# Kernel tuning notes

Measured on AMD Instinct MI355X. Metric: run time of the kernel, lower is better.

## Reference

```python
import jax, jax.numpy as jnp
import numpy as np

N_HEAD = 16

def setup_inputs() -> dict:
    key = jax.random.key(0)
    k1, k2, k3 = jax.random.split(key, 3)
    B, T, D = 1, 2048, 1024
    x = jax.random.normal(k1, (B, T, D), dtype=jnp.float32)
    # torch Linear(d, 3d, bias=False): y = x @ W.T with W [3d, d]; store transposed [d, 3d]
    W_qkv = jax.random.normal(k2, (D, 3 * D), dtype=jnp.float32) * 0.02
    W_o = jax.random.normal(k3, (D, D), dtype=jnp.float32) * 0.02
    return {"x": x, "W_qkv": W_qkv, "W_o": W_o}

def reference(x, W_qkv, W_o):
    B, T, D = x.shape
    H = N_HEAD
    hd = D // H
    qkv = (x @ W_qkv).reshape(B, T, 3, H, hd)
    q, k, v = qkv[:, :, 0], qkv[:, :, 1], qkv[:, :, 2]  # [B, T, H, hd]
    scale = 1.0 / np.sqrt(hd).astype(np.float32)
    # The per-chunk loop with growing context + mask is exactly dense causal attention.
    att = jnp.einsum('bqhd,bkhd->bhqk', q, k) * scale  # [B, H, T, T]
    causal = jnp.tril(jnp.ones((T, T), dtype=bool))
    att = jnp.where(causal[None, None], att, jnp.finfo(att.dtype).min)
    att = jax.nn.softmax(att, axis=-1)
    y = jnp.einsum('bhqk,bkhd->bqhd', att, v).reshape(B, T, D)
    return y @ W_o
```

## Files before the change

kernel.cpp:

```cpp
#include <hip/hip_runtime.h>
#include <hip/hip_bf16.h>


using u16 = unsigned short;
typedef __attribute__((ext_vector_type(8))) __bf16 bf16x8;
typedef __attribute__((ext_vector_type(8))) unsigned short u16x8;
typedef __attribute__((ext_vector_type(4))) float f32x4;

__device__ __forceinline__ u16 f2bf(float f) {
  union { float f; unsigned u; } v; v.f = f;
  unsigned r = v.u + 0x7FFFu + ((v.u >> 16) & 1u);
  return (u16)(r >> 16);
}

__device__ __forceinline__ float bf2f(u16 b) {
  union { unsigned u; float f; } v; v.u = ((unsigned)b) << 16;
  return v.f;
}

__device__ __forceinline__ unsigned cvt_pk_bf16(float lo, float hi) {
  unsigned r;
  asm("v_cvt_pk_bf16_f32 %0, %1, %2" : "=v"(r) : "v"(lo), "v"(hi));
  return r;
}

__device__ __forceinline__ void gload_lds16(const void* g, void* l) {
  __builtin_amdgcn_global_load_lds((const __attribute__((address_space(1))) void*)g,
                                   (__attribute__((address_space(3))) void*)l, 16, 0, 0);
}

__device__ __forceinline__ f32x4 mfma16(bf16x8 a, bf16x8 b, f32x4 c) {
  return __builtin_amdgcn_mfma_f32_16x16x32_bf16(a, b, c, 0, 0, 0);
}

__global__ __launch_bounds__(256) void prep_kernel(const float* __restrict__ x,
                                                   const float* __restrict__ Wqkv,
                                                   const float* __restrict__ Wo,
                                                   u16* __restrict__ xb,
                                                   u16* __restrict__ WqkvT,
                                                   u16* __restrict__ WoT) {
  __shared__ u16 tile[32][33];
  const int b = blockIdx.x;
  if (b < 1024) {
    const int i = (b * 256 + threadIdx.x) * 8;
    float4 a = *(const float4*)(x + i);
    float4 c = *(const float4*)(x + i + 4);
    u16x8 r;
    r[0] = f2bf(a.x); r[1] = f2bf(a.y); r[2] = f2bf(a.z); r[3] = f2bf(a.w);
    r[4] = f2bf(c.x); r[5] = f2bf(c.y); r[6] = f2bf(c.z); r[7] = f2bf(c.w);
    *(u16x8*)(xb + i) = r;
    return;
  }
  const float* in; u16* out; int R, C, bx, by;
  if (b < 1024 + 3072) {
    const int tb = b - 1024;
    in = Wqkv; out = WqkvT; R = 1024; C = 3072; bx = tb % 96; by = tb / 96;
  } else {
    const int tb = b - 4096;
    in = Wo; out = WoT; R = 1024; C = 1024; bx = tb % 32; by = tb / 32;
  }
  const int c0 = bx * 32, r0 = by * 32;
  const int tx = threadIdx.x & 31, ty = threadIdx.x >> 5;
#pragma unroll
  for (int rr = ty; rr < 32; rr += 8)
    tile[rr][tx] = f2bf(in[(size_t)(r0 + rr) * C + (c0 + tx)]);
  __syncthreads();
#pragma unroll
  for (int rr = ty; rr < 32; rr += 8)
    out[(size_t)(c0 + rr) * R + (r0 + tx)] = tile[tx][rr];
}

template <int BN, typename OutT>
__global__ __launch_bounds__(256) void gemm_bt_kernel(const u16* __restrict__ A,
                                                      const u16* __restrict__ Bt,
                                                      OutT* __restrict__ C,
                                                      int M, int N, int K) {
  constexpr int BM = 128, BK = 32;
  constexpr int NFR = BN / 32;
  __shared__ u16 As[2][BM * BK];
  __shared__ u16 Bs[2][BN * BK];
  const int tid = threadIdx.x;
  const int lane = tid & 63, wid = tid >> 6;
  const int l16 = lane & 15, l4 = lane >> 4;
  const int wr = (wid >> 1) * 64, wc = (wid & 1) * (BN / 2);
  const long bm = (long)blockIdx.x * BM, bn = (long)blockIdx.y * BN;

  f32x4 acc[4][NFR] = {};
  const int KT = K / BK;

  auto stage = [&](int buf, int kt) {
    const int k0 = kt * BK;
#pragma unroll
    for (int half = 0; half < 2; ++half) {
      int t = half * 256 + tid;
      int row = t >> 2, c8 = (t & 3) << 3;
      gload_lds16(A + (bm + row) * (size_t)K + k0 + c8, &As[buf][row * BK + c8]);
    }
#pragma unroll
    for (int half = 0; half < 2; ++half) {
      int t = half * 256 + tid;
      if (t < BN * 4) {
        int row = t >> 2, c8 = (t & 3) << 3;
        gload_lds16(Bt + (bn + row) * (size_t)K + k0 + c8, &Bs[buf][row * BK + c8]);
      }
    }
  };

  stage(0, 0);
  __syncthreads();
  int cur = 0;
  for (int kt = 0; kt < KT; ++kt) {
    if (kt + 1 < KT) stage(cur ^ 1, kt + 1);
    bf16x8 af[4], bfr[NFR];
#pragma unroll
    for (int m = 0; m < 4; ++m)
      af[m] = *(const bf16x8*)&As[cur][(wr + m * 16 + l16) * BK + l4 * 8];
#pragma unroll
    for (int n = 0; n < NFR; ++n)
      bfr[n] = *(const bf16x8*)&Bs[cur][(wc + n * 16 + l16) * BK + l4 * 8];
#pragma unroll
    for (int m = 0; m < 4; ++m)
#pragma unroll
      for (int n = 0; n < NFR; ++n)
        acc[m][n] = mfma16(af[m], bfr[n], acc[m][n]);
    __syncthreads();
    cur ^= 1;
  }

#pragma unroll
  for (int m = 0; m < 4; ++m) {
    const long row0 = bm + wr + m * 16 + l4 * 4;
#pragma unroll
    for (int n = 0; n < NFR; ++n) {
      const long col = bn + wc + n * 16 + l16;
#pragma unroll
      for (int j = 0; j < 4; ++j) {
        float v = acc[m][n][j];
        if constexpr (sizeof(OutT) == 2)
          C[(row0 + j) * N + col] = (OutT)f2bf(v);
        else
          C[(row0 + j) * N + col] = (OutT)v;
      }
    }
  }
}

__global__ __launch_bounds__(256, 4) void attn_kernel(const u16* __restrict__ qkv,
                                                      u16* __restrict__ opart,
                                                      float2* __restrict__ ml, int S) {
  constexpr int W = 3072;
  const int p = blockIdx.x, h = blockIdx.y, s = blockIdx.z;
  const int tid = threadIdx.x, wid = tid >> 6, lane = tid & 63;
  const int l16 = lane & 15, l4 = lane >> 4;
  const int w0 = (33 * s) / S, w1 = (33 * (s + 1)) / S;

  __shared__ u16 Ks[2][64 * 64];
  __shared__ u16 Vt[2][64][72];

  constexpr float cl2 = 0.125f * 1.44269504f;
  constexpr float MFIX = 12.0f;
  const int vpos = (lane & 32) | ((lane & 12) << 1) | ((lane & 16) >> 2) | (lane & 3);

  auto stageK = [&](int buf, int k0) {
#pragma unroll
    for (int half = 0; half < 2; ++half) {
      int t = half * 256 + tid;
      int row = t >> 3, chunk = t & 7;
      int srcChunk = chunk ^ (row & 7);
      gload_lds16(qkv + (size_t)(k0 + row) * W + 1024 + h * 64 + srcChunk * 8,
                  &Ks[buf][t * 8]);
    }
  };

  bool didA = false, didB = false;
  int w = w0;
  while (w < w1) {
    const bool isA = (w <= p);
    const int qt = isA ? p : 31 - p;
    const int wend = isA ? ((w1 < p + 1) ? w1 : (p + 1)) : w1;
    const int kvb = isA ? 0 : p + 1;
    if (isA) didA = true; else didB = true;

    const int q0 = qt * 64;
    const int qr = q0 + wid * 16 + l16;

    const u16* qrow = qkv + (size_t)(q0 + wid * 16 + l16) * W + h * 64;
    const bf16x8 qa0 = *(const bf16x8*)(qrow + l4 * 8);
    const bf16x8 qa1 = *(const bf16x8*)(qrow + 32 + l4 * 8);

    f32x4 o[4] = {};
    float lsum = 0.f;

    {
      const int k0 = (w - kvb) * 64;
      stageK(0, k0);
      const u16* vsrc = qkv + (size_t)(k0 + lane) * W + 2048 + h * 64 + wid * 16;
      u16x8 a = *(const u16x8*)vsrc;
      u16x8 b = *(const u16x8*)(vsrc + 8);
#pragma unroll
      for (int i = 0; i < 8; ++i) Vt[0][wid * 16 + i][vpos] = a[i];
#pragma unroll
      for (int i = 0; i < 8; ++i) Vt[0][wid * 16 + 8 + i][vpos] = b[i];
      __syncthreads();
    }

    int cur = 0;
    for (; w < wend; ++w) {
      const int kv = w - kvb;
      const int k0 = kv * 64;
      const bool pf = (w + 1 < wend);

      u16x8 va, vb2;
      if (pf) {
        stageK(cur ^ 1, k0 + 64);
        const u16* vsrc = qkv + (size_t)(k0 + 64 + lane) * W + 2048 + h * 64 + wid * 16;
        va = *(const u16x8*)vsrc;
        vb2 = *(const u16x8*)(vsrc + 8);
      }

      f32x4 sv[4];
#pragma unroll
      for (int nb = 0; nb < 4; ++nb) {
        const int krow = nb * 16 + l16;
        const char* kbase = (const char*)&Ks[cur][0] + krow * 128;
        const int swz = (krow & 7) << 4;
        bf16x8 kb0 = *(const bf16x8*)(kbase + ((l4 * 16) ^ swz));
        bf16x8 kb1 = *(const bf16x8*)(kbase + ((64 + l4 * 16) ^ swz));
        f32x4 z = {0.f, 0.f, 0.f, 0.f};
        z = mfma16(kb0, qa0, z);
        sv[nb] = mfma16(kb1, qa1, z);
      }

      float pv[4][4];
      const bool diag = (kv == qt);
#pragma unroll
      for (int nb = 0; nb < 4; ++nb)
#pragma unroll
        for (int j = 0; j < 4; ++j) {
          float e = exp2f(fmaf(sv[nb][j], cl2, -MFIX));
          if (diag) {
            const int key = k0 + nb * 16 + l4 * 4 + j;
            e = (key <= qr) ? e : 0.f;
          }
          pv[nb][j] = e;
          lsum += e;
        }

      uint4 pk0, pk1;
      pk0.x = cvt_pk_bf16(pv[0][0], pv[0][1]);
      pk0.y = cvt_pk_bf16(pv[0][2], pv[0][3]);
      pk0.z = cvt_pk_bf16(pv[1][0], pv[1][1]);
      pk0.w = cvt_pk_bf16(pv[1][2], pv[1][3]);
      pk1.x = cvt_pk_bf16(pv[2][0], pv[2][1]);
      pk1.y = cvt_pk_bf16(pv[2][2], pv[2][3]);
      pk1.z = cvt_pk_bf16(pv[3][0], pv[3][1]);
      pk1.w = cvt_pk_bf16(pv[3][2], pv[3][3]);

#pragma unroll
      for (int db = 0; db < 4; ++db) {
        bf16x8 va0 = *(const bf16x8*)&Vt[cur][db * 16 + l16][l4 * 8];
        bf16x8 va1 = *(const bf16x8*)&Vt[cur][db * 16 + l16][32 + l4 * 8];
        o[db] = mfma16(va0, *(const bf16x8*)&pk0, o[db]);
        o[db] = mfma16(va1, *(const bf16x8*)&pk1, o[db]);
      }

      if (pf) {
#pragma unroll
        for (int i = 0; i < 8; ++i) Vt[cur ^ 1][wid * 16 + i][vpos] = va[i];
#pragma unroll
        for (int i = 0; i < 8; ++i) Vt[cur ^ 1][wid * 16 + 8 + i][vpos] = vb2[i];
      }
      __syncthreads();
      cur ^= 1;
    }

    float lrow = lsum;
    lrow += __shfl_xor(lrow, 16);
    lrow += __shfl_xor(lrow, 32);
    {
      const size_t q = q0 + wid * 16 + l16;
      u16* orow = opart + ((q * 16 + h) * S + s) * 64;
#pragma unroll
      for (int db = 0; db < 4; ++db) {
        uint2 w2;
        w2.x = cvt_pk_bf16(o[db][0], o[db][1]);
        w2.y = cvt_pk_bf16(o[db][2], o[db][3]);
        *(uint2*)&orow[db * 16 + l4 * 4] = w2;
      }
      if (l4 == 0)
        ml[(q * 16 + h) * S + s] = make_float2(MFIX, lrow);
    }
    lsum = 0.f;
  }

  if (!didA && tid < 64)
    ml[((size_t)(p * 64 + tid) * 16 + h) * S + s] = make_float2(-3e38f, 0.f);
  if (!didB && tid < 64)
    ml[((size_t)((31 - p) * 64 + tid) * 16 + h) * S + s] = make_float2(-3e38f, 0.f);
}

__global__ __launch_bounds__(256) void combine_kernel(const u16* __restrict__ opart,
                                                      const float2* __restrict__ ml,
                                                      u16* __restrict__ y, int S) {
  const int p = blockIdx.x * 4 + (threadIdx.x >> 6);
  const int d = threadIdx.x & 63;
  float M = -3e38f;
  for (int s = 0; s < S; ++s) M = fmaxf(M, ml[(size_t)p * S + s].x);
  float num = 0.f, den = 0.f;
  for (int s = 0; s < S; ++s) {
    const float2 m2 = ml[(size_t)p * S + s];
    const float w = exp2f(m2.x - M);
    num += w * bf2f(opart[((size_t)p * S + s) * 64 + d]);
    den += w * m2.y;
  }
  const int q = p >> 4, h = p & 15;
  y[(size_t)q * 1024 + h * 64 + d] = f2bf(num / den);
}

extern "C" void kernel_launch(void* const* d_in, const int* in_sizes, int n_in,
                              void* d_out, int out_size, void* d_ws, size_t ws_size,
                              hipStream_t stream) {
  constexpr int T = 2048, D = 1024;
  const float* x    = (const float*)d_in[0];
  const float* Wqkv = (const float*)d_in[1];
  const float* Wo   = (const float*)d_in[2];
  float* out = (float*)d_out;

  u16* xb    = (u16*)d_ws;
  u16* WqkvT = xb + (size_t)T * D;
  u16* WoT   = WqkvT + (size_t)3 * D * D;
  u16* qkv   = WoT + (size_t)D * D;
  u16* yb    = qkv + (size_t)T * 3 * D;

  const size_t baseB = (size_t)(T * D + 3 * D * D + D * D + T * 3 * D + T * D) * 2;
  auto needB = [&](int S) {
    return baseB + (size_t)T * 16 * S * 64 * 2 + (size_t)T * 16 * S * 8;
  };
  const int S = (ws_size >= needB(4)) ? 4 : 2;
  u16*    opart = (u16*)((char*)d_ws + baseB);
  float2* ml    = (float2*)((char*)d_ws + baseB + (size_t)T * 16 * S * 64 * 2);

  prep_kernel<<<1024 + 3072 + 1024, 256, 0, stream>>>(x, Wqkv, Wo, xb, WqkvT, WoT);

  gemm_bt_kernel<96, u16><<<dim3(T / 128, 3 * D / 96), 256, 0, stream>>>(
      xb, WqkvT, qkv, T, 3 * D, D);

  attn_kernel<<<dim3(16, 16, S), 256, 0, stream>>>(qkv, opart, ml, S);
  combine_kernel<<<T * 16 / 4, 256, 0, stream>>>(opart, ml, yb, S);

  gemm_bt_kernel<64, float><<<dim3(T / 128, D / 64), 256, 0, stream>>>(
      yb, WoT, out, T, D, D);
}
```

Measured before the change: 97.06 us.

## Split attention key tiles across two wave groups with LDS reduction

The attention block grows from 4 to 8 waves. Each pair of waves shares the same 16 query rows and splits the 64-key tile into two 32-key halves. Staging of K and V is spread over 512 threads, so each thread loads half as much. At the end, the partial outputs and row sums are combined through shared memory that reuses the K/V buffers. This aims to raise wave-level parallelism and latency hiding in the attention kernel, at the cost of an extra barrier, an LDS reduction per query tile, and more register pressure under launch bounds of 512 threads with a minimum of 8 blocks.

```diff
diff --git a/kernel.cpp b/kernel.cpp
--- a/kernel.cpp
+++ b/kernel.cpp
@@ -145,12 +145,13 @@
   }
 }
 
-__global__ __launch_bounds__(256, 4) void attn_kernel(const u16* __restrict__ qkv,
+__global__ __launch_bounds__(512, 8) void attn_kernel(const u16* __restrict__ qkv,
                                                       u16* __restrict__ opart,
                                                       float2* __restrict__ ml, int S) {
   constexpr int W = 3072;
   const int p = blockIdx.x, h = blockIdx.y, s = blockIdx.z;
-  const int tid = threadIdx.x, wid = tid >> 6, lane = tid & 63;
+  const int tid = threadIdx.x, lane = tid & 63;
+  const int qsub = (tid >> 6) & 3, khalf = tid >> 8;
   const int l16 = lane & 15, l4 = lane >> 4;
   const int w0 = (33 * s) / S, w1 = (33 * (s + 1)) / S;
 
@@ -159,17 +160,14 @@
 
   constexpr float cl2 = 0.125f * 1.44269504f;
   constexpr float MFIX = 12.0f;
-  const int vpos = (lane & 32) | ((lane & 12) << 1) | ((lane & 16) >> 2) | (lane & 3);
+  const int vkey = tid & 63, vdg = tid >> 6;
+  const int vpos = (vkey & 32) | ((vkey & 12) << 1) | ((vkey & 16) >> 2) | (vkey & 3);
 
   auto stageK = [&](int buf, int k0) {
-#pragma unroll
-    for (int half = 0; half < 2; ++half) {
-      int t = half * 256 + tid;
-      int row = t >> 3, chunk = t & 7;
-      int srcChunk = chunk ^ (row & 7);
-      gload_lds16(qkv + (size_t)(k0 + row) * W + 1024 + h * 64 + srcChunk * 8,
-                  &Ks[buf][t * 8]);
-    }
+    const int row = tid >> 3, chunk = tid & 7;
+    const int srcChunk = chunk ^ (row & 7);
+    gload_lds16(qkv + (size_t)(k0 + row) * W + 1024 + h * 64 + srcChunk * 8,
+                &Ks[buf][tid * 8]);
   };
 
   bool didA = false, didB = false;
@@ -182,25 +180,23 @@
     if (isA) didA = true; else didB = true;
 
     const int q0 = qt * 64;
-    const int qr = q0 + wid * 16 + l16;
-
-    const u16* qrow = qkv + (size_t)(q0 + wid * 16 + l16) * W + h * 64;
+    const int qr = q0 + qsub * 16 + l16;
+
+    const u16* qrow = qkv + (size_t)(q0 + qsub * 16 + l16) * W + h * 64;
     const bf16x8 qa0 = *(const bf16x8*)(qrow + l4 * 8);
     const bf16x8 qa1 = *(const bf16x8*)(qrow + 32 + l4 * 8);
 
     f32x4 o[4] = {};
     float lsum = 0.f;
 
+    __syncthreads();
     {
       const int k0 = (w - kvb) * 64;
       stageK(0, k0);
-      const u16* vsrc = qkv + (size_t)(k0 + lane) * W + 2048 + h * 64 + wid * 16;
+      const u16* vsrc = qkv + (size_t)(k0 + vkey) * W + 2048 + h * 64 + vdg * 8;
       u16x8 a = *(const u16x8*)vsrc;
-      u16x8 b = *(const u16x8*)(vsrc + 8);
-#pragma unroll
-      for (int i = 0; i < 8; ++i) Vt[0][wid * 16 + i][vpos] = a[i];
-#pragma unroll
-      for (int i = 0; i < 8; ++i) Vt[0][wid * 16 + 8 + i][vpos] = b[i];
+#pragma unroll
+      for (int i = 0; i < 8; ++i) Vt[0][vdg * 8 + i][vpos] = a[i];
       __syncthreads();
     }
 
@@ -210,18 +206,16 @@
       const int k0 = kv * 64;
       const bool pf = (w + 1 < wend);
 
-      u16x8 va, vb2;
+      u16x8 va8;
       if (pf) {
         stageK(cur ^ 1, k0 + 64);
-        const u16* vsrc = qkv + (size_t)(k0 + 64 + lane) * W + 2048 + h * 64 + wid * 16;
-        va = *(const u16x8*)vsrc;
-        vb2 = *(const u16x8*)(vsrc + 8);
-      }
-
-      f32x4 sv[4];
-#pragma unroll
-      for (int nb = 0; nb < 4; ++nb) {
-        const int krow = nb * 16 + l16;
+        va8 = *(const u16x8*)(qkv + (size_t)(k0 + 64 + vkey) * W + 2048 + h * 64 + vdg * 8);
+      }
+
+      f32x4 sv[2];
+#pragma unroll
+      for (int nb = 0; nb < 2; ++nb) {
+        const int krow = khalf * 32 + nb * 16 + l16;
         const char* kbase = (const char*)&Ks[cur][0] + krow * 128;
         const int swz = (krow & 7) << 4;
         bf16x8 kb0 = *(const bf16x8*)(kbase + ((l4 * 16) ^ swz));
@@ -231,44 +225,36 @@
         sv[nb] = mfma16(kb1, qa1, z);
       }
 
-      float pv[4][4];
+      float pv[2][4];
       const bool diag = (kv == qt);
 #pragma unroll
-      for (int nb = 0; nb < 4; ++nb)
+      for (int nb = 0; nb < 2; ++nb)
 #pragma unroll
         for (int j = 0; j < 4; ++j) {
           float e = exp2f(fmaf(sv[nb][j], cl2, -MFIX));
           if (diag) {
-            const int key = k0 + nb * 16 + l4 * 4 + j;
+            const int key = k0 + khalf * 32 + nb * 16 + l4 * 4 + j;
             e = (key <= qr) ? e : 0.f;
           }
           pv[nb][j] = e;
           lsum += e;
         }
 
-      uint4 pk0, pk1;
-      pk0.x = cvt_pk_bf16(pv[0][0], pv[0][1]);
-      pk0.y = cvt_pk_bf16(pv[0][2], pv[0][3]);
-      pk0.z = cvt_pk_bf16(pv[1][0], pv[1][1]);
-      pk0.w = cvt_pk_bf16(pv[1][2], pv[1][3]);
-      pk1.x = cvt_pk_bf16(pv[2][0], pv[2][1]);
-      pk1.y = cvt_pk_bf16(pv[2][2], pv[2][3]);
-      pk1.z = cvt_pk_bf16(pv[3][0], pv[3][1]);
-      pk1.w = cvt_pk_bf16(pv[3][2], pv[3][3]);
+      uint4 pk;
+      pk.x = cvt_pk_bf16(pv[0][0], pv[0][1]);
+      pk.y = cvt_pk_bf16(pv[0][2], pv[0][3]);
+      pk.z = cvt_pk_bf16(pv[1][0], pv[1][1]);
+      pk.w = cvt_pk_bf16(pv[1][2], pv[1][3]);
 
 #pragma unroll
       for (int db = 0; db < 4; ++db) {
-        bf16x8 va0 = *(const bf16x8*)&Vt[cur][db * 16 + l16][l4 * 8];
-        bf16x8 va1 = *(const bf16x8*)&Vt[cur][db * 16 + l16][32 + l4 * 8];
-        o[db] = mfma16(va0, *(const bf16x8*)&pk0, o[db]);
-        o[db] = mfma16(va1, *(const bf16x8*)&pk1, o[db]);
+        bf16x8 va = *(const bf16x8*)&Vt[cur][db * 16 + l16][khalf * 32 + l4 * 8];
+        o[db] = mfma16(va, *(const bf16x8*)&pk, o[db]);
       }
 
       if (pf) {
 #pragma unroll
-        for (int i = 0; i < 8; ++i) Vt[cur ^ 1][wid * 16 + i][vpos] = va[i];
-#pragma unroll
-        for (int i = 0; i < 8; ++i) Vt[cur ^ 1][wid * 16 + 8 + i][vpos] = vb2[i];
+        for (int i = 0; i < 8; ++i) Vt[cur ^ 1][vdg * 8 + i][vpos] = va8[i];
       }
       __syncthreads();
       cur ^= 1;
@@ -277,8 +263,25 @@
     float lrow = lsum;
     lrow += __shfl_xor(lrow, 16);
     lrow += __shfl_xor(lrow, 32);
-    {
-      const size_t q = q0 + wid * 16 + l16;
+    float* Osc = (float*)&Ks[0][0];
+    float* lsc = (float*)&Vt[0][0][0];
+    if (khalf == 1) {
+#pragma unroll
+      for (int db = 0; db < 4; ++db)
+#pragma unroll
+        for (int j = 0; j < 4; ++j)
+          Osc[((qsub * 64 + db * 16 + l4 * 4 + j) << 4) + l16] = o[db][j];
+      if (l4 == 0) lsc[qsub * 16 + l16] = lrow;
+    }
+    __syncthreads();
+    if (khalf == 0) {
+#pragma unroll
+      for (int db = 0; db < 4; ++db)
+#pragma unroll
+        for (int j = 0; j < 4; ++j)
+          o[db][j] += Osc[((qsub * 64 + db * 16 + l4 * 4 + j) << 4) + l16];
+      lrow += lsc[qsub * 16 + l16];
+      const size_t q = q0 + qsub * 16 + l16;
       u16* orow = opart + ((q * 16 + h) * S + s) * 64;
 #pragma unroll
       for (int db = 0; db < 4; ++db) {
@@ -290,7 +293,6 @@
       if (l4 == 0)
         ml[(q * 16 + h) * S + s] = make_float2(MFIX, lrow);
     }
-    lsum = 0.f;
   }
 
   if (!didA && tid < 64)
@@ -345,7 +347,7 @@
   gemm_bt_kernel<96, u16><<<dim3(T / 128, 3 * D / 96), 256, 0, stream>>>(
       xb, WqkvT, qkv, T, 3 * D, D);
 
-  attn_kernel<<<dim3(16, 16, S), 256, 0, stream>>>(qkv, opart, ml, S);
+  attn_kernel<<<dim3(16, 16, S), 512, 0, stream>>>(qkv, opart, ml, S);
   combine_kernel<<<T * 16 / 4, 256, 0, stream>>>(opart, ml, yb, S);
 
   gemm_bt_kernel<64, float><<<dim3(T / 128, D / 64), 256, 0, stream>>>(
```

After: 105.3 us. 8.5% more time.
